# Performance work log

Hardware: AMD Instinct MI355X
Metric: run time of the kernel (lower is better)

## Reference

```python
import jax, jax.numpy as jnp
import numpy as np

N, B, E = 50000, 1, 800000
D_IN = 128      # input_size == out_size (residual)
HID = 128       # hidden_size
H = 4           # heads
C = HID // H    # per-head dim = 32
EPS = 1e-5


def setup_inputs() -> dict:
    key = jax.random.key(0)
    ks = jax.random.split(key, 16)
    s_in = 1.0 / np.sqrt(D_IN)
    s_hid = 1.0 / np.sqrt(HID)
    return {
        "x": jax.random.normal(ks[0], (N, B, D_IN), jnp.float32),
        "edge_index": jax.random.randint(ks[1], (2, E), 0, N, jnp.int64 if jax.config.jax_enable_x64 else jnp.int32),
        "edge_attr": jax.random.normal(ks[2], (E, HID), jnp.float32),
        # TransformerConv projections (weights stored torch-style [out, in])
        "Wq": jax.random.uniform(ks[3], (HID, D_IN), jnp.float32, -s_in, s_in),
        "bq": jnp.zeros((HID,), jnp.float32),
        "Wk": jax.random.uniform(ks[4], (HID, D_IN), jnp.float32, -s_in, s_in),
        "bk": jnp.zeros((HID,), jnp.float32),
        "Wv": jax.random.uniform(ks[5], (HID, D_IN), jnp.float32, -s_in, s_in),
        "bv": jnp.zeros((HID,), jnp.float32),
        "We": jax.random.uniform(ks[6], (HID, HID), jnp.float32, -s_hid, s_hid),  # lin_edge, no bias
        "Wskip": jax.random.uniform(ks[7], (HID, D_IN), jnp.float32, -s_in, s_in),
        "bskip": jnp.zeros((HID,), jnp.float32),
        "Wp": jax.random.uniform(ks[8], (HID, HID), jnp.float32, -s_hid, s_hid),   # physics_linear
        "bp": jnp.zeros((HID,), jnp.float32),
        "Wm": jax.random.uniform(ks[9], (D_IN, HID), jnp.float32, -s_hid, s_hid),  # merge_linear
        "bm": jnp.zeros((D_IN,), jnp.float32),
    }


def reference(x, edge_index, edge_attr, Wq, bq, Wk, bk, Wv, bv, We,
              Wskip, bskip, Wp, bp, Wm, bm):
    n = x.shape[0]
    src, dst = edge_index[0], edge_index[1]  # message flows src -> dst (j -> i)

    # node-wise QKV projections -> [N, B, H, C]
    q = (x @ Wq.T + bq).reshape(n, B, H, C)
    k = (x @ Wk.T + bk).reshape(n, B, H, C)
    v = (x @ Wv.T + bv).reshape(n, B, H, C)

    # edge feature projection -> [E, H, C]
    e = (edge_attr @ We.T).reshape(-1, H, C)

    # per-edge attention scores [E, B, H]
    k_j = k[src] + e[:, None]                       # [E, B, H, C]
    alpha = (q[dst] * k_j).sum(-1) / jnp.sqrt(jnp.asarray(C, x.dtype))

    # scatter-softmax over incoming edges of each dst node
    m = jax.ops.segment_max(alpha, dst, num_segments=n)      # [N, B, H]
    a = jnp.exp(alpha - m[dst])
    s = jax.ops.segment_sum(a, dst, num_segments=n)
    alpha = a / s[dst]

    # weighted scatter-add aggregation
    msg = (v[src] + e[:, None]) * alpha[..., None]           # [E, B, H, C]
    out = jax.ops.segment_sum(msg, dst, num_segments=n)      # [N, B, H, C]
    out = out.reshape(n, B, H * C)

    # root skip connection
    out = out + (x @ Wskip.T + bskip)

    # GraphResidualBlock tail
    out = jax.nn.relu(out)
    out = out @ Wp.T + bp
    # custom LayerNorm: normalize over the node dim (dim 0), weight/bias unused
    mu = out.mean(0, keepdims=True)
    sd = out.std(0, keepdims=True)
    out = (out - mu) / (sd + EPS)
    out = jax.nn.relu(out)
    out = out @ Wm.T + bm
    return out + x
```

## Files before the change

### kernel.cpp

```cpp
#include <hip/hip_runtime.h>
#include <stdint.h>

#define RS32 0.17677669529663687f
#define LDW 40

typedef short bf16x8 __attribute__((ext_vector_type(8)));
typedef float f32x4 __attribute__((ext_vector_type(4)));

__device__ __forceinline__ ushort f2bf(float f) {
  uint32_t b = __float_as_uint(f);
  b = (b + 0x7fffu + ((b >> 16) & 1u)) >> 16;
  return (ushort)b;
}
__device__ __forceinline__ float bflo(uint32_t w) { return __uint_as_float(w << 16); }
__device__ __forceinline__ float bfhi(uint32_t w) { return __uint_as_float(w & 0xffff0000u); }

__device__ __forceinline__ void stage16(ushort* hiA, ushort* loA, int r, int koff,
                                        const float* v) {
  uint32_t hu[8], lu[8];
#pragma unroll
  for (int i = 0; i < 8; ++i) {
    uint32_t b0 = __float_as_uint(v[2 * i]), b1 = __float_as_uint(v[2 * i + 1]);
    uint32_t h0m = b0 & 0xffff0000u, h1m = b1 & 0xffff0000u;
    hu[i] = (b0 >> 16) | h1m;
    float l0 = v[2 * i] - __uint_as_float(h0m);
    float l1 = v[2 * i + 1] - __uint_as_float(h1m);
    lu[i] = (__float_as_uint(l0) >> 16) | (__float_as_uint(l1) & 0xffff0000u);
  }
  *(uint4*)&hiA[r * LDW + koff]     = make_uint4(hu[0], hu[1], hu[2], hu[3]);
  *(uint4*)&hiA[r * LDW + koff + 8] = make_uint4(hu[4], hu[5], hu[6], hu[7]);
  *(uint4*)&loA[r * LDW + koff]     = make_uint4(lu[0], lu[1], lu[2], lu[3]);
  *(uint4*)&loA[r * LDW + koff + 8] = make_uint4(lu[4], lu[5], lu[6], lu[7]);
}

__launch_bounds__(256)
__global__ void gemm128_mfma_kernel(int mode,
                                    const float* __restrict__ A, const float* __restrict__ A2,
                                    const float* __restrict__ W, const float* __restrict__ bias,
                                    const float* __restrict__ mu, const float* __restrict__ inv,
                                    const float* __restrict__ X, float* __restrict__ out,
                                    float* __restrict__ sums, float* __restrict__ sumsq, int N)
{
  __shared__ ushort Ahi[128 * LDW], Alo[128 * LDW], Whi[128 * LDW], Wlo[128 * LDW];
  const int tid = threadIdx.x;
  const int nb = blockIdx.x * 128;
  const int lane = tid & 63, wv = tid >> 6;
  const int wr = (wv >> 1) * 64, wc = (wv & 1) * 64;
  const int fr = lane & 15, fq = lane >> 4;
  const int sr = tid >> 1, sk = (tid & 1) * 16;

  f32x4 acc[4][4];
#pragma unroll
  for (int m = 0; m < 4; ++m)
#pragma unroll
    for (int n = 0; n < 4; ++n) acc[m][n] = (f32x4)0.0f;

  for (int kc = 0; kc < 128; kc += 32) {
    float va[16], vw[16];
    {
      int gr = nb + sr;
      if (gr < N) {
#pragma unroll
        for (int i = 0; i < 4; ++i) {
          float4 v = *(const float4*)(A + (size_t)gr * 128 + kc + sk + i * 4);
          if (mode == 1) {
            float4 b = *(const float4*)(A2 + (size_t)gr * 128 + kc + sk + i * 4);
            v.x = fmaxf(v.x + b.x, 0.f); v.y = fmaxf(v.y + b.y, 0.f);
            v.z = fmaxf(v.z + b.z, 0.f); v.w = fmaxf(v.w + b.w, 0.f);
          } else if (mode == 2) {
            float4 m4 = *(const float4*)(mu + kc + sk + i * 4);
            float4 i4 = *(const float4*)(inv + kc + sk + i * 4);
            v.x = fmaxf((v.x - m4.x) * i4.x, 0.f); v.y = fmaxf((v.y - m4.y) * i4.y, 0.f);
            v.z = fmaxf((v.z - m4.z) * i4.z, 0.f); v.w = fmaxf((v.w - m4.w) * i4.w, 0.f);
          }
          va[i * 4 + 0] = v.x; va[i * 4 + 1] = v.y; va[i * 4 + 2] = v.z; va[i * 4 + 3] = v.w;
        }
      } else {
#pragma unroll
        for (int i = 0; i < 16; ++i) va[i] = 0.f;
      }
#pragma unroll
      for (int i = 0; i < 4; ++i) {
        float4 v = *(const float4*)(W + (size_t)sr * 128 + kc + sk + i * 4);
        vw[i * 4 + 0] = v.x; vw[i * 4 + 1] = v.y; vw[i * 4 + 2] = v.z; vw[i * 4 + 3] = v.w;
      }
    }
    if (kc) __syncthreads();
    stage16(Ahi, Alo, sr, sk, va);
    stage16(Whi, Wlo, sr, sk, vw);
    __syncthreads();

    bf16x8 ah[4], al[4], bh[4], bl[4];
#pragma unroll
    for (int m = 0; m < 4; ++m) {
      const int row = wr + m * 16 + fr;
      ah[m] = *(const bf16x8*)&Ahi[row * LDW + fq * 8];
      al[m] = *(const bf16x8*)&Alo[row * LDW + fq * 8];
    }
#pragma unroll
    for (int n = 0; n < 4; ++n) {
      const int col = wc + n * 16 + fr;
      bh[n] = *(const bf16x8*)&Whi[col * LDW + fq * 8];
      bl[n] = *(const bf16x8*)&Wlo[col * LDW + fq * 8];
    }
#pragma unroll
    for (int m = 0; m < 4; ++m)
#pragma unroll
      for (int n = 0; n < 4; ++n) {
        acc[m][n] = __builtin_amdgcn_mfma_f32_16x16x32_bf16(ah[m], bh[n], acc[m][n], 0, 0, 0);
        acc[m][n] = __builtin_amdgcn_mfma_f32_16x16x32_bf16(al[m], bh[n], acc[m][n], 0, 0, 0);
        acc[m][n] = __builtin_amdgcn_mfma_f32_16x16x32_bf16(ah[m], bl[n], acc[m][n], 0, 0, 0);
      }
  }

  float bcol[4];
#pragma unroll
  for (int n = 0; n < 4; ++n) bcol[n] = bias[wc + n * 16 + fr];
  float csum[4] = {0.f, 0.f, 0.f, 0.f}, csum2[4] = {0.f, 0.f, 0.f, 0.f};
#pragma unroll
  for (int m = 0; m < 4; ++m) {
    const int r0 = nb + wr + m * 16 + fq * 4;
#pragma unroll
    for (int r = 0; r < 4; ++r) {
      const int gr = r0 + r;
      if (gr < N) {
#pragma unroll
        for (int n = 0; n < 4; ++n) {
          const int c = wc + n * 16 + fr;
          float o = acc[m][n][r] + bcol[n];
          if (mode == 2) o += X[(size_t)gr * 128 + c];
          out[(size_t)gr * 128 + c] = o;
          if (mode == 1) { csum[n] += o; csum2[n] = fmaf(o, o, csum2[n]); }
        }
      }
    }
  }
  if (mode == 1) {
#pragma unroll
    for (int n = 0; n < 4; ++n) {
      csum[n] += __shfl_xor(csum[n], 16, 64);
      csum[n] += __shfl_xor(csum[n], 32, 64);
      csum2[n] += __shfl_xor(csum2[n], 16, 64);
      csum2[n] += __shfl_xor(csum2[n], 32, 64);
    }
    if (fq == 0) {
#pragma unroll
      for (int n = 0; n < 4; ++n) {
        atomicAdd(&sums[wc + n * 16 + fr], csum[n]);
        atomicAdd(&sumsq[wc + n * 16 + fr], csum2[n]);
      }
    }
  }
}

__launch_bounds__(256)
__global__ void proj_direct_kernel(const ushort* __restrict__ xb16,
                                   const ushort* __restrict__ Wb,
                                   const ushort* __restrict__ Mtb,
                                   const float* __restrict__ bk, const float* __restrict__ bv,
                                   const float* __restrict__ bs, const float* __restrict__ bq,
                                   const float* __restrict__ bu,
                                   float* __restrict__ os, ushort* __restrict__ kvi,
                                   ushort* __restrict__ u, ushort* __restrict__ qb, int N)
{
  const int y = blockIdx.y;
  const ushort* Wsrc = (y < 4) ? (Wb + (size_t)y * 16384) : (Mtb + (size_t)(y - 4) * 16384);

  const int tid = threadIdx.x;
  const int nb = blockIdx.x * 128;
  const int lane = tid & 63, wv = tid >> 6;
  const int wr = (wv >> 1) * 64, wc = (wv & 1) * 64;
  const int fr = lane & 15, fq = lane >> 4;

  f32x4 acc[4][4];
#pragma unroll
  for (int m = 0; m < 4; ++m)
#pragma unroll
    for (int n = 0; n < 4; ++n) acc[m][n] = (f32x4)0.0f;

#pragma unroll
  for (int kk = 0; kk < 4; ++kk) {
    const int ko = kk * 32 + fq * 8;
    bf16x8 af[4], bf[4];
#pragma unroll
    for (int m = 0; m < 4; ++m)
      af[m] = *(const bf16x8*)(xb16 + (size_t)(nb + wr + m * 16 + fr) * 128 + ko);
#pragma unroll
    for (int n = 0; n < 4; ++n)
      bf[n] = *(const bf16x8*)(Wsrc + (size_t)(wc + n * 16 + fr) * 128 + ko);
#pragma unroll
    for (int m = 0; m < 4; ++m)
#pragma unroll
      for (int n = 0; n < 4; ++n)
        acc[m][n] = __builtin_amdgcn_mfma_f32_16x16x32_bf16(af[m], bf[n], acc[m][n], 0, 0, 0);
  }

  float bcol[4];
#pragma unroll
  for (int n = 0; n < 4; ++n) {
    const int c = wc + n * 16 + fr;
    bcol[n] = (y == 0) ? bk[c] : (y == 1) ? bv[c] : (y == 2) ? bs[c]
            : (y == 3) ? bq[c] : bu[(y - 4) * 128 + c];
  }
#pragma unroll
  for (int m = 0; m < 4; ++m) {
    const int r0 = nb + wr + m * 16 + fq * 4;
#pragma unroll
    for (int r = 0; r < 4; ++r) {
      const int gr = r0 + r;
      if (gr < N) {
#pragma unroll
        for (int n = 0; n < 4; ++n) {
          const int c = wc + n * 16 + fr;
          float o = acc[m][n][r] + bcol[n];
          if (y == 2)      os[(size_t)gr * 128 + c] = o;
          else if (y == 3) qb[(size_t)gr * 128 + c] = f2bf(o);
          else if (y == 0) kvi[(size_t)gr * 256 + (c >> 2) * 8 + (c & 3)] = f2bf(o);
          else if (y == 1) kvi[(size_t)gr * 256 + (c >> 2) * 8 + 4 + (c & 3)] = f2bf(o);
          else             u[(size_t)gr * 512 + (y - 4) * 128 + c] = f2bf(o);
        }
      }
    }
  }
}

__global__ void x2bf_kernel(const float* __restrict__ x, ushort* __restrict__ xb, int total4)
{
  int i = blockIdx.x * 256 + threadIdx.x;
  if (i < total4) {
    float4 v = ((const float4*)x)[i];
    uint2 w = make_uint2((uint32_t)f2bf(v.x) | ((uint32_t)f2bf(v.y) << 16),
                         (uint32_t)f2bf(v.z) | ((uint32_t)f2bf(v.w) << 16));
    ((uint2*)xb)[i] = w;
  }
}

__global__ void prep_wb_kernel(const float* __restrict__ Wk, const float* __restrict__ Wv,
                               const float* __restrict__ Ws, const float* __restrict__ Wq,
                               ushort* __restrict__ Wb)
{
  int i = blockIdx.x * 256 + threadIdx.x;
  if (i >= 4 * 16384) return;
  int y = i >> 14, r = i & 16383;
  const float* src = (y == 0) ? Wk : (y == 1) ? Wv : (y == 2) ? Ws : Wq;
  Wb[i] = f2bf(src[r]);
}

__global__ void prep_mt_kernel(const float* __restrict__ Wq, const float* __restrict__ We,
                               ushort* __restrict__ Mtb)
{
  const int tid = threadIdx.x;
  const int jp = blockIdx.x * 2 + (tid >> 7);
  const int d = tid & 127;
  const int h = jp >> 7, j = jp & 127;
  const float* wq = Wq + (size_t)(32 * h) * 128 + d;
  const float* we = We + (size_t)(32 * h) * 128 + j;
  float acc = 0.f;
#pragma unroll 8
  for (int a = 0; a < 32; ++a) acc = fmaf(wq[a * 128], we[a * 128], acc);
  Mtb[(size_t)jp * 128 + d] = f2bf(acc);
}

__global__ void prep_bu_kernel(const float* __restrict__ bq, const float* __restrict__ We,
                               float* __restrict__ bu)
{
  const int jp = threadIdx.x;
  const int h = jp >> 7, j = jp & 127;
  float acc = 0.f;
  for (int a = 0; a < 32; ++a)
    acc = fmaf(bq[32 * h + a], We[(size_t)(32 * h + a) * 128 + j], acc);
  bu[jp] = acc;
}

__global__ void prep_web_kernel(const float* __restrict__ We, ushort* __restrict__ WeB)
{
  int idx = blockIdx.x * 256 + threadIdx.x;
  if (idx >= 128 * 512) return;
  int c = idx >> 9, j = idx & 511;
  int hh = j >> 7, k2 = j & 127;
  WeB[idx] = (hh == (c >> 5)) ? f2bf(We[(size_t)c * 128 + k2]) : (ushort)0;
}

__global__ void deg_kernel(const int* __restrict__ ei, int* __restrict__ deg, int E)
{
  int e = blockIdx.x * 256 + threadIdx.x;
  if (e < E) atomicAdd(&deg[ei[E + e]], 1);
}

__launch_bounds__(256)
__global__ void start_kernel(const int* __restrict__ deg, int* __restrict__ offs,
                             int* __restrict__ cursor, int* __restrict__ gcount, int N)
{
  const int i = blockIdx.x * 256 + threadIdx.x;
  const int lane = threadIdx.x & 63;
  int d = (i < N) ? deg[i] : 0;
  int scan = d;
#pragma unroll
  for (int ofs = 1; ofs < 64; ofs <<= 1) {
    int t = __shfl_up(scan, ofs, 64);
    if (lane >= ofs) scan += t;
  }
  int total = __shfl(scan, 63, 64);
  int base = 0;
  if (lane == 63) base = atomicAdd(gcount, total);
  base = __shfl(base, 63, 64);
  int excl = base + scan - d;
  if (i < N) { offs[i] = excl; cursor[i] = excl; }
}

__global__ void fill_kernel(const int* __restrict__ ei, int* __restrict__ cursor,
                            int2* __restrict__ csr, int E)
{
  int e = blockIdx.x * 256 + threadIdx.x;
  if (e < E) {
    int dst = ei[E + e];
    int slot = atomicAdd(&cursor[dst], 1);
    csr[slot] = make_int2(ei[e], e);
  }
}

__launch_bounds__(256)
__global__ void fused_attn2_kernel(const int2* __restrict__ csr, const int* __restrict__ offs,
                                   const int* __restrict__ deg,
                                   const ushort* __restrict__ qb, const ushort* __restrict__ kvi,
                                   const ushort* __restrict__ u,
                                   const float* __restrict__ eattr,
                                   ushort* __restrict__ aggS, float* __restrict__ wsS, int N)
{
  const int tid = threadIdx.x;
  const int lane = tid & 63;
  const int wid = tid >> 6;
  const int p = lane >> 5;
  const int j32 = lane & 31;
  const int c0 = j32 * 4;
  const int h = j32 >> 3;
  const int gwave = blockIdx.x * 4 + wid;
  const int nwaves = gridDim.x * 4;

  for (int n = gwave; n < N; n += nwaves) {
    const int e0 = offs[n];
    const int e1 = e0 + deg[n];

    const uint2 qp = *(const uint2*)(qb + (size_t)n * 128 + c0);
    uint2 uhp[4];
#pragma unroll
    for (int hh = 0; hh < 4; ++hh)
      uhp[hh] = *(const uint2*)(u + (size_t)n * 512 + hh * 128 + c0);

    float ws0 = 0.f, ws1 = 0.f, ws2 = 0.f, ws3 = 0.f;
    float ax[4][4];
#pragma unroll
    for (int hh = 0; hh < 4; ++hh)
#pragma unroll
      for (int j = 0; j < 4; ++j) ax[hh][j] = 0.f;
    float sm0 = 0.f, sm1 = 0.f, sm2 = 0.f, sm3 = 0.f;

    int sl = e0 + p;
    if (sl < e1) {
      int2 seC = csr[sl];
      float4 eaC = *(const float4*)(eattr + (size_t)seC.y * 128 + c0);
      uint4 kvC = *(const uint4*)(kvi + (size_t)seC.x * 256 + j32 * 8);
      int sln = sl + 2;
      int2 seN = (sln < e1) ? csr[sln] : seC;
      for (; sl < e1; sl += 2) {
        float4 eaN = *(const float4*)(eattr + (size_t)seN.y * 128 + c0);
        uint4 kvN = *(const uint4*)(kvi + (size_t)seN.x * 256 + j32 * 8);
        const int slf = sl + 4;
        int2 seF = (slf < e1) ? csr[slf] : seN;

        float P0 = eaC.x * bflo(uhp[0].x) + eaC.y * bfhi(uhp[0].x)
                 + eaC.z * bflo(uhp[0].y) + eaC.w * bfhi(uhp[0].y);
        float P1 = eaC.x * bflo(uhp[1].x) + eaC.y * bfhi(uhp[1].x)
                 + eaC.z * bflo(uhp[1].y) + eaC.w * bfhi(uhp[1].y);
        float P2 = eaC.x * bflo(uhp[2].x) + eaC.y * bfhi(uhp[2].x)
                 + eaC.z * bflo(uhp[2].y) + eaC.w * bfhi(uhp[2].y);
        float P3 = eaC.x * bflo(uhp[3].x) + eaC.y * bfhi(uhp[3].x)
                 + eaC.z * bflo(uhp[3].y) + eaC.w * bfhi(uhp[3].y);
        const float qk = bflo(qp.x) * bflo(kvC.x) + bfhi(qp.x) * bfhi(kvC.x)
                       + bflo(qp.y) * bflo(kvC.y) + bfhi(qp.y) * bfhi(kvC.y);
        P0 += (h == 0) ? qk : 0.f;
        P1 += (h == 1) ? qk : 0.f;
        P2 += (h == 2) ? qk : 0.f;
        P3 += (h == 3) ? qk : 0.f;
#pragma unroll
        for (int mm = 1; mm <= 16; mm <<= 1) {
          P0 += __shfl_xor(P0, mm, 64);
          P1 += __shfl_xor(P1, mm, 64);
          P2 += __shfl_xor(P2, mm, 64);
          P3 += __shfl_xor(P3, mm, 64);
        }
        const float a0 = __expf(P0 * RS32);
        const float a1 = __expf(P1 * RS32);
        const float a2 = __expf(P2 * RS32);
        const float a3 = __expf(P3 * RS32);
        sm0 += a0; sm1 += a1; sm2 += a2; sm3 += a3;
        const float aV = (h == 0) ? a0 : (h == 1) ? a1 : (h == 2) ? a2 : a3;
        ws0 = fmaf(aV, bflo(kvC.z), ws0); ws1 = fmaf(aV, bfhi(kvC.z), ws1);
        ws2 = fmaf(aV, bflo(kvC.w), ws2); ws3 = fmaf(aV, bfhi(kvC.w), ws3);
        ax[0][0] = fmaf(a0, eaC.x, ax[0][0]); ax[0][1] = fmaf(a0, eaC.y, ax[0][1]);
        ax[0][2] = fmaf(a0, eaC.z, ax[0][2]); ax[0][3] = fmaf(a0, eaC.w, ax[0][3]);
        ax[1][0] = fmaf(a1, eaC.x, ax[1][0]); ax[1][1] = fmaf(a1, eaC.y, ax[1][1]);
        ax[1][2] = fmaf(a1, eaC.z, ax[1][2]); ax[1][3] = fmaf(a1, eaC.w, ax[1][3]);
        ax[2][0] = fmaf(a2, eaC.x, ax[2][0]); ax[2][1] = fmaf(a2, eaC.y, ax[2][1]);
        ax[2][2] = fmaf(a2, eaC.z, ax[2][2]); ax[2][3] = fmaf(a2, eaC.w, ax[2][3]);
        ax[3][0] = fmaf(a3, eaC.x, ax[3][0]); ax[3][1] = fmaf(a3, eaC.y, ax[3][1]);
        ax[3][2] = fmaf(a3, eaC.z, ax[3][2]); ax[3][3] = fmaf(a3, eaC.w, ax[3][3]);

        eaC = eaN; kvC = kvN; seN = seF;
      }
    }

#pragma unroll
    for (int hh = 0; hh < 4; ++hh)
#pragma unroll
      for (int j = 0; j < 4; ++j) ax[hh][j] += __shfl_xor(ax[hh][j], 32, 64);
    ws0 += __shfl_xor(ws0, 32, 64); ws1 += __shfl_xor(ws1, 32, 64);
    ws2 += __shfl_xor(ws2, 32, 64); ws3 += __shfl_xor(ws3, 32, 64);
    sm0 += __shfl_xor(sm0, 32, 64); sm1 += __shfl_xor(sm1, 32, 64);
    sm2 += __shfl_xor(sm2, 32, 64); sm3 += __shfl_xor(sm3, 32, 64);

    const float iv0 = (sm0 > 0.f) ? 1.f / sm0 : 0.f;
    const float iv1 = (sm1 > 0.f) ? 1.f / sm1 : 0.f;
    const float iv2 = (sm2 > 0.f) ? 1.f / sm2 : 0.f;
    const float iv3 = (sm3 > 0.f) ? 1.f / sm3 : 0.f;

    if (p == 0) {
      const float s = (h == 0) ? iv0 : (h == 1) ? iv1 : (h == 2) ? iv2 : iv3;
      *(float4*)(wsS + (size_t)n * 128 + c0) =
          make_float4(ws0 * s, ws1 * s, ws2 * s, ws3 * s);
    }

    float o0[4], o1[4], s0, s1;
    if (p == 0) {
#pragma unroll
      for (int j = 0; j < 4; ++j) { o0[j] = ax[0][j]; o1[j] = ax[1][j]; }
      s0 = iv0; s1 = iv1;
    } else {
#pragma unroll
      for (int j = 0; j < 4; ++j) { o0[j] = ax[2][j]; o1[j] = ax[3][j]; }
      s0 = iv2; s1 = iv3;
    }
    uint2 w0 = make_uint2(((uint32_t)f2bf(o0[0] * s0)) | (((uint32_t)f2bf(o0[1] * s0)) << 16),
                          ((uint32_t)f2bf(o0[2] * s0)) | (((uint32_t)f2bf(o0[3] * s0)) << 16));
    uint2 w1 = make_uint2(((uint32_t)f2bf(o1[0] * s1)) | (((uint32_t)f2bf(o1[1] * s1)) << 16),
                          ((uint32_t)f2bf(o1[2] * s1)) | (((uint32_t)f2bf(o1[3] * s1)) << 16));
    *(uint2*)(aggS + (size_t)n * 512 + (p * 2) * 128 + c0) = w0;
    *(uint2*)(aggS + (size_t)n * 512 + (p * 2 + 1) * 128 + c0) = w1;
  }
}

__launch_bounds__(256)
__global__ void agg_gemm_kernel(const ushort* __restrict__ aggS, const ushort* __restrict__ WeB,
                                const float* __restrict__ wsX, float* __restrict__ attn, int N)
{
  __shared__ ushort As[128][72];
  __shared__ ushort Bs[128][72];
  const int tid = threadIdx.x;
  const int nb = blockIdx.x * 128;
  const int lane = tid & 63, wv = tid >> 6;
  const int wr = (wv >> 1) * 64, wc = (wv & 1) * 64;
  const int fr = lane & 15, fq = lane >> 4;
  const int r = tid >> 1, cs = (tid & 1) * 32;

  f32x4 acc[4][4];
#pragma unroll
  for (int m = 0; m < 4; ++m)
#pragma unroll
    for (int n = 0; n < 4; ++n) acc[m][n] = (f32x4)0.0f;

  for (int kc = 0; kc < 512; kc += 64) {
    uint4 av[4], bv[4];
    if (nb + r < N) {
      const uint4* src = (const uint4*)(aggS + (size_t)(nb + r) * 512 + kc + cs);
      av[0] = src[0]; av[1] = src[1]; av[2] = src[2]; av[3] = src[3];
    } else {
#pragma unroll
      for (int i = 0; i < 4; ++i) av[i] = make_uint4(0, 0, 0, 0);
    }
    {
      const uint4* src = (const uint4*)(WeB + (size_t)r * 512 + kc + cs);
      bv[0] = src[0]; bv[1] = src[1]; bv[2] = src[2]; bv[3] = src[3];
    }
    if (kc) __syncthreads();
#pragma unroll
    for (int i = 0; i < 4; ++i) {
      *(uint4*)&As[r][cs + i * 8] = av[i];
      *(uint4*)&Bs[r][cs + i * 8] = bv[i];
    }
    __syncthreads();

#pragma unroll
    for (int s = 0; s < 2; ++s) {
      bf16x8 ah[4], bh[4];
#pragma unroll
      for (int m = 0; m < 4; ++m)
        ah[m] = *(const bf16x8*)&As[wr + m * 16 + fr][s * 32 + fq * 8];
#pragma unroll
      for (int n = 0; n < 4; ++n)
        bh[n] = *(const bf16x8*)&Bs[wc + n * 16 + fr][s * 32 + fq * 8];
#pragma unroll
      for (int m = 0; m < 4; ++m)
#pragma unroll
        for (int n = 0; n < 4; ++n)
          acc[m][n] = __builtin_amdgcn_mfma_f32_16x16x32_bf16(ah[m], bh[n], acc[m][n], 0, 0, 0);
    }
  }

#pragma unroll
  for (int m = 0; m < 4; ++m) {
    const int r0 = nb + wr + m * 16 + fq * 4;
#pragma unroll
    for (int rr = 0; rr < 4; ++rr) {
      const int gr = r0 + rr;
      if (gr < N) {
#pragma unroll
        for (int n = 0; n < 4; ++n) {
          const int c = wc + n * 16 + fr;
          attn[(size_t)gr * 128 + c] = acc[m][n][rr] + wsX[(size_t)gr * 128 + c];
        }
      }
    }
  }
}

__global__ void finalize_stats_kernel(const float* __restrict__ sums, const float* __restrict__ sumsq,
                                      float* __restrict__ mu, float* __restrict__ inv, int N)
{
  int c = threadIdx.x;
  float m = sums[c] / (float)N;
  float var = sumsq[c] / (float)N - m * m;
  float sd = sqrtf(fmaxf(var, 0.f));
  mu[c] = m;
  inv[c] = 1.f / (sd + 1e-5f);
}

extern "C" void kernel_launch(void* const* d_in, const int* in_sizes, int n_in,
                              void* d_out, int out_size, void* d_ws, size_t ws_size,
                              hipStream_t stream) {
  const float* x    = (const float*)d_in[0];
  const int*   ei   = (const int*)d_in[1];
  const float* eatt = (const float*)d_in[2];
  const float* Wq = (const float*)d_in[3];  const float* bq = (const float*)d_in[4];
  const float* Wk = (const float*)d_in[5];  const float* bk = (const float*)d_in[6];
  const float* Wv = (const float*)d_in[7];  const float* bv = (const float*)d_in[8];
  const float* We = (const float*)d_in[9];
  const float* Wsk = (const float*)d_in[10]; const float* bsk = (const float*)d_in[11];
  const float* Wp = (const float*)d_in[12]; const float* bp = (const float*)d_in[13];
  const float* Wm = (const float*)d_in[14]; const float* bm = (const float*)d_in[15];
  float* out = (float*)d_out;

  const int N = in_sizes[0] / 128;
  const int E = in_sizes[1] / 2;

  char* w = (char*)d_ws;
  auto alloc = [&](size_t bytes) {
    char* p = w;
    w += (bytes + 255) & ~(size_t)255;
    return p;
  };
  const size_t node_f = (size_t)N * 128 * sizeof(float);
  float*  skip = (float*)alloc(node_f);
  float*  wsA  = (float*)alloc(node_f);
  float*  t1   = (float*)alloc(node_f);
  ushort* xb16 = (ushort*)alloc((size_t)N * 128 * sizeof(ushort));
  ushort* qb   = (ushort*)alloc((size_t)N * 128 * sizeof(ushort));
  ushort* kvi  = (ushort*)alloc((size_t)N * 256 * sizeof(ushort));
  ushort* u    = (ushort*)alloc((size_t)N * 512 * sizeof(ushort));
  ushort* aggS = (ushort*)alloc((size_t)N * 512 * sizeof(ushort));
  ushort* WeB  = (ushort*)alloc(128 * 512 * sizeof(ushort));
  ushort* Wb   = (ushort*)alloc(4 * 128 * 128 * sizeof(ushort));
  ushort* Mtb  = (ushort*)alloc(512 * 128 * sizeof(ushort));
  float*  bu   = (float*)alloc(512 * sizeof(float));
  int*    deg  = (int*)alloc((size_t)N * sizeof(int));
  int*    offs = (int*)alloc((size_t)N * sizeof(int));
  int*    curs = (int*)alloc((size_t)N * sizeof(int));
  int*    gcnt = (int*)alloc(sizeof(int));
  int2*   csr  = (int2*)alloc((size_t)E * sizeof(int2));
  float*  sums  = (float*)alloc(128 * sizeof(float));
  float*  sumsq = (float*)alloc(128 * sizeof(float));
  float*  mu    = (float*)alloc(128 * sizeof(float));
  float*  inv   = (float*)alloc(128 * sizeof(float));
  (void)ws_size; (void)n_in; (void)out_size;

  const int NB = (N + 127) / 128;
  const int EB = (E + 255) / 256;

  hipMemsetAsync(deg, 0, (size_t)N * sizeof(int), stream);
  hipMemsetAsync(gcnt, 0, sizeof(int), stream);
  hipMemsetAsync(sums, 0, 2 * 128 * sizeof(float), stream);

  x2bf_kernel<<<(N * 32 + 255) / 256, 256, 0, stream>>>(x, xb16, N * 32);
  prep_wb_kernel<<<256, 256, 0, stream>>>(Wk, Wv, Wsk, Wq, Wb);
  prep_mt_kernel<<<256, 256, 0, stream>>>(Wq, We, Mtb);
  prep_bu_kernel<<<1, 512, 0, stream>>>(bq, We, bu);
  prep_web_kernel<<<256, 256, 0, stream>>>(We, WeB);

  proj_direct_kernel<<<dim3(NB, 8), 256, 0, stream>>>(xb16, Wb, Mtb, bk, bv, bsk, bq, bu,
                                                      skip, kvi, u, qb, N);

  deg_kernel<<<EB, 256, 0, stream>>>(ei, deg, E);
  start_kernel<<<(N + 255) / 256, 256, 0, stream>>>(deg, offs, curs, gcnt, N);
  fill_kernel<<<EB, 256, 0, stream>>>(ei, curs, csr, E);

  fused_attn2_kernel<<<2048, 256, 0, stream>>>(csr, offs, deg, qb, kvi, u, eatt,
                                               aggS, wsA, N);

  agg_gemm_kernel<<<NB, 256, 0, stream>>>(aggS, WeB, wsA, wsA, N);

  gemm128_mfma_kernel<<<NB, 256, 0, stream>>>(1, wsA, skip, Wp, bp, nullptr, nullptr, nullptr,
                                              t1, sums, sumsq, N);
  finalize_stats_kernel<<<1, 128, 0, stream>>>(sums, sumsq, mu, inv, N);

  gemm128_mfma_kernel<<<NB, 256, 0, stream>>>(2, t1, nullptr, Wm, bm, mu, inv, x, out,
                                              nullptr, nullptr, N);
}
```

Measured before the change: 517.7 us.

## Fuse aggregation GEMM with physics linear and drop split-bf16 tail GEMMs

Fuses the edge-aggregation GEMM with the residual add, skip add, ReLU and the physics_linear GEMM plus column statistics into one kernel. The ReLU output stays in shared memory, so the float intermediate never round-trips through global memory. The skip projection is now stored as bf16. The tail GEMMs drop the hi/lo split-bf16 three-MFMA scheme for a single bf16 MFMA, with a separate kernel that normalizes and casts the second input to bf16. This cuts memory traffic and MFMA work at the cost of lower precision (plain bf16 operands) in the tail.

```diff
diff --git a/kernel.cpp b/kernel.cpp
--- a/kernel.cpp
+++ b/kernel.cpp
@@ -2,7 +2,6 @@
 #include <stdint.h>
 
 #define RS32 0.17677669529663687f
-#define LDW 40
 
 typedef short bf16x8 __attribute__((ext_vector_type(8)));
 typedef float f32x4 __attribute__((ext_vector_type(4)));
@@ -14,144 +13,7 @@
 }
 __device__ __forceinline__ float bflo(uint32_t w) { return __uint_as_float(w << 16); }
 __device__ __forceinline__ float bfhi(uint32_t w) { return __uint_as_float(w & 0xffff0000u); }
-
-__device__ __forceinline__ void stage16(ushort* hiA, ushort* loA, int r, int koff,
-                                        const float* v) {
-  uint32_t hu[8], lu[8];
-#pragma unroll
-  for (int i = 0; i < 8; ++i) {
-    uint32_t b0 = __float_as_uint(v[2 * i]), b1 = __float_as_uint(v[2 * i + 1]);
-    uint32_t h0m = b0 & 0xffff0000u, h1m = b1 & 0xffff0000u;
-    hu[i] = (b0 >> 16) | h1m;
-    float l0 = v[2 * i] - __uint_as_float(h0m);
-    float l1 = v[2 * i + 1] - __uint_as_float(h1m);
-    lu[i] = (__float_as_uint(l0) >> 16) | (__float_as_uint(l1) & 0xffff0000u);
-  }
-  *(uint4*)&hiA[r * LDW + koff]     = make_uint4(hu[0], hu[1], hu[2], hu[3]);
-  *(uint4*)&hiA[r * LDW + koff + 8] = make_uint4(hu[4], hu[5], hu[6], hu[7]);
-  *(uint4*)&loA[r * LDW + koff]     = make_uint4(lu[0], lu[1], lu[2], lu[3]);
-  *(uint4*)&loA[r * LDW + koff + 8] = make_uint4(lu[4], lu[5], lu[6], lu[7]);
-}
-
-__launch_bounds__(256)
-__global__ void gemm128_mfma_kernel(int mode,
-                                    const float* __restrict__ A, const float* __restrict__ A2,
-                                    const float* __restrict__ W, const float* __restrict__ bias,
-                                    const float* __restrict__ mu, const float* __restrict__ inv,
-                                    const float* __restrict__ X, float* __restrict__ out,
-                                    float* __restrict__ sums, float* __restrict__ sumsq, int N)
-{
-  __shared__ ushort Ahi[128 * LDW], Alo[128 * LDW], Whi[128 * LDW], Wlo[128 * LDW];
-  const int tid = threadIdx.x;
-  const int nb = blockIdx.x * 128;
-  const int lane = tid & 63, wv = tid >> 6;
-  const int wr = (wv >> 1) * 64, wc = (wv & 1) * 64;
-  const int fr = lane & 15, fq = lane >> 4;
-  const int sr = tid >> 1, sk = (tid & 1) * 16;
-
-  f32x4 acc[4][4];
-#pragma unroll
-  for (int m = 0; m < 4; ++m)
-#pragma unroll
-    for (int n = 0; n < 4; ++n) acc[m][n] = (f32x4)0.0f;
-
-  for (int kc = 0; kc < 128; kc += 32) {
-    float va[16], vw[16];
-    {
-      int gr = nb + sr;
-      if (gr < N) {
-#pragma unroll
-        for (int i = 0; i < 4; ++i) {
-          float4 v = *(const float4*)(A + (size_t)gr * 128 + kc + sk + i * 4);
-          if (mode == 1) {
-            float4 b = *(const float4*)(A2 + (size_t)gr * 128 + kc + sk + i * 4);
-            v.x = fmaxf(v.x + b.x, 0.f); v.y = fmaxf(v.y + b.y, 0.f);
-            v.z = fmaxf(v.z + b.z, 0.f); v.w = fmaxf(v.w + b.w, 0.f);
-          } else if (mode == 2) {
-            float4 m4 = *(const float4*)(mu + kc + sk + i * 4);
-            float4 i4 = *(const float4*)(inv + kc + sk + i * 4);
-            v.x = fmaxf((v.x - m4.x) * i4.x, 0.f); v.y = fmaxf((v.y - m4.y) * i4.y, 0.f);
-            v.z = fmaxf((v.z - m4.z) * i4.z, 0.f); v.w = fmaxf((v.w - m4.w) * i4.w, 0.f);
-          }
-          va[i * 4 + 0] = v.x; va[i * 4 + 1] = v.y; va[i * 4 + 2] = v.z; va[i * 4 + 3] = v.w;
-        }
-      } else {
-#pragma unroll
-        for (int i = 0; i < 16; ++i) va[i] = 0.f;
-      }
-#pragma unroll
-      for (int i = 0; i < 4; ++i) {
-        float4 v = *(const float4*)(W + (size_t)sr * 128 + kc + sk + i * 4);
-        vw[i * 4 + 0] = v.x; vw[i * 4 + 1] = v.y; vw[i * 4 + 2] = v.z; vw[i * 4 + 3] = v.w;
-      }
-    }
-    if (kc) __syncthreads();
-    stage16(Ahi, Alo, sr, sk, va);
-    stage16(Whi, Wlo, sr, sk, vw);
-    __syncthreads();
-
-    bf16x8 ah[4], al[4], bh[4], bl[4];
-#pragma unroll
-    for (int m = 0; m < 4; ++m) {
-      const int row = wr + m * 16 + fr;
-      ah[m] = *(const bf16x8*)&Ahi[row * LDW + fq * 8];
-      al[m] = *(const bf16x8*)&Alo[row * LDW + fq * 8];
-    }
-#pragma unroll
-    for (int n = 0; n < 4; ++n) {
-      const int col = wc + n * 16 + fr;
-      bh[n] = *(const bf16x8*)&Whi[col * LDW + fq * 8];
-      bl[n] = *(const bf16x8*)&Wlo[col * LDW + fq * 8];
-    }
-#pragma unroll
-    for (int m = 0; m < 4; ++m)
-#pragma unroll
-      for (int n = 0; n < 4; ++n) {
-        acc[m][n] = __builtin_amdgcn_mfma_f32_16x16x32_bf16(ah[m], bh[n], acc[m][n], 0, 0, 0);
-        acc[m][n] = __builtin_amdgcn_mfma_f32_16x16x32_bf16(al[m], bh[n], acc[m][n], 0, 0, 0);
-        acc[m][n] = __builtin_amdgcn_mfma_f32_16x16x32_bf16(ah[m], bl[n], acc[m][n], 0, 0, 0);
-      }
-  }
-
-  float bcol[4];
-#pragma unroll
-  for (int n = 0; n < 4; ++n) bcol[n] = bias[wc + n * 16 + fr];
-  float csum[4] = {0.f, 0.f, 0.f, 0.f}, csum2[4] = {0.f, 0.f, 0.f, 0.f};
-#pragma unroll
-  for (int m = 0; m < 4; ++m) {
-    const int r0 = nb + wr + m * 16 + fq * 4;
-#pragma unroll
-    for (int r = 0; r < 4; ++r) {
-      const int gr = r0 + r;
-      if (gr < N) {
-#pragma unroll
-        for (int n = 0; n < 4; ++n) {
-          const int c = wc + n * 16 + fr;
-          float o = acc[m][n][r] + bcol[n];
-          if (mode == 2) o += X[(size_t)gr * 128 + c];
-          out[(size_t)gr * 128 + c] = o;
-          if (mode == 1) { csum[n] += o; csum2[n] = fmaf(o, o, csum2[n]); }
-        }
-      }
-    }
-  }
-  if (mode == 1) {
-#pragma unroll
-    for (int n = 0; n < 4; ++n) {
-      csum[n] += __shfl_xor(csum[n], 16, 64);
-      csum[n] += __shfl_xor(csum[n], 32, 64);
-      csum2[n] += __shfl_xor(csum2[n], 16, 64);
-      csum2[n] += __shfl_xor(csum2[n], 32, 64);
-    }
-    if (fq == 0) {
-#pragma unroll
-      for (int n = 0; n < 4; ++n) {
-        atomicAdd(&sums[wc + n * 16 + fr], csum[n]);
-        atomicAdd(&sumsq[wc + n * 16 + fr], csum2[n]);
-      }
-    }
-  }
-}
+__device__ __forceinline__ float bfu(ushort s) { return __uint_as_float(((uint32_t)s) << 16); }
 
 __launch_bounds__(256)
 __global__ void proj_direct_kernel(const ushort* __restrict__ xb16,
@@ -160,7 +22,7 @@
                                    const float* __restrict__ bk, const float* __restrict__ bv,
                                    const float* __restrict__ bs, const float* __restrict__ bq,
                                    const float* __restrict__ bu,
-                                   float* __restrict__ os, ushort* __restrict__ kvi,
+                                   ushort* __restrict__ skipb, ushort* __restrict__ kvi,
                                    ushort* __restrict__ u, ushort* __restrict__ qb, int N)
 {
   const int y = blockIdx.y;
@@ -213,7 +75,7 @@
         for (int n = 0; n < 4; ++n) {
           const int c = wc + n * 16 + fr;
           float o = acc[m][n][r] + bcol[n];
-          if (y == 2)      os[(size_t)gr * 128 + c] = o;
+          if (y == 2)      skipb[(size_t)gr * 128 + c] = f2bf(o);
           else if (y == 3) qb[(size_t)gr * 128 + c] = f2bf(o);
           else if (y == 0) kvi[(size_t)gr * 256 + (c >> 2) * 8 + (c & 3)] = f2bf(o);
           else if (y == 1) kvi[(size_t)gr * 256 + (c >> 2) * 8 + 4 + (c & 3)] = f2bf(o);
@@ -244,6 +106,13 @@
   int y = i >> 14, r = i & 16383;
   const float* src = (y == 0) ? Wk : (y == 1) ? Wv : (y == 2) ? Ws : Wq;
   Wb[i] = f2bf(src[r]);
+}
+
+__global__ void prep_w2_kernel(const float* __restrict__ Wp, const float* __restrict__ Wm,
+                               ushort* __restrict__ Wpb, ushort* __restrict__ Wmb)
+{
+  int i = blockIdx.x * 256 + threadIdx.x;
+  if (i < 16384) { Wpb[i] = f2bf(Wp[i]); Wmb[i] = f2bf(Wm[i]); }
 }
 
 __global__ void prep_mt_kernel(const float* __restrict__ Wq, const float* __restrict__ We,
@@ -450,11 +319,15 @@
 }
 
 __launch_bounds__(256)
-__global__ void agg_gemm_kernel(const ushort* __restrict__ aggS, const ushort* __restrict__ WeB,
-                                const float* __restrict__ wsX, float* __restrict__ attn, int N)
-{
-  __shared__ ushort As[128][72];
-  __shared__ ushort Bs[128][72];
+__global__ void fused_post_kernel(const ushort* __restrict__ aggS, const ushort* __restrict__ WeB,
+                                  const float* __restrict__ wsS, const ushort* __restrict__ skipb,
+                                  const ushort* __restrict__ Wpb, const float* __restrict__ bp,
+                                  float* __restrict__ t1,
+                                  float* __restrict__ sums, float* __restrict__ sumsq, int N)
+{
+  __shared__ ushort smem[2 * 128 * 72];
+  ushort* As = smem;
+  ushort* Bs = smem + 128 * 72;
   const int tid = threadIdx.x;
   const int nb = blockIdx.x * 128;
   const int lane = tid & 63, wv = tid >> 6;
@@ -484,8 +357,8 @@
     if (kc) __syncthreads();
 #pragma unroll
     for (int i = 0; i < 4; ++i) {
-      *(uint4*)&As[r][cs + i * 8] = av[i];
-      *(uint4*)&Bs[r][cs + i * 8] = bv[i];
+      *(uint4*)&As[r * 72 + cs + i * 8] = av[i];
+      *(uint4*)&Bs[r * 72 + cs + i * 8] = bv[i];
     }
     __syncthreads();
 
@@ -494,10 +367,10 @@
       bf16x8 ah[4], bh[4];
 #pragma unroll
       for (int m = 0; m < 4; ++m)
-        ah[m] = *(const bf16x8*)&As[wr + m * 16 + fr][s * 32 + fq * 8];
+        ah[m] = *(const bf16x8*)&As[(wr + m * 16 + fr) * 72 + s * 32 + fq * 8];
 #pragma unroll
       for (int n = 0; n < 4; ++n)
-        bh[n] = *(const bf16x8*)&Bs[wc + n * 16 + fr][s * 32 + fq * 8];
+        bh[n] = *(const bf16x8*)&Bs[(wc + n * 16 + fr) * 72 + s * 32 + fq * 8];
 #pragma unroll
       for (int m = 0; m < 4; ++m)
 #pragma unroll
@@ -505,7 +378,56 @@
           acc[m][n] = __builtin_amdgcn_mfma_f32_16x16x32_bf16(ah[m], bh[n], acc[m][n], 0, 0, 0);
     }
   }
-
+  __syncthreads();
+
+  ushort* zs = smem;
+#pragma unroll
+  for (int m = 0; m < 4; ++m) {
+    const int lr0 = wr + m * 16 + fq * 4;
+#pragma unroll
+    for (int rr = 0; rr < 4; ++rr) {
+      const int lrow = lr0 + rr;
+      const int gr = nb + lrow;
+#pragma unroll
+      for (int n = 0; n < 4; ++n) {
+        const int c = wc + n * 16 + fr;
+        float o = 0.f;
+        if (gr < N) {
+          o = acc[m][n][rr] + wsS[(size_t)gr * 128 + c] + bfu(skipb[(size_t)gr * 128 + c]);
+          o = fmaxf(o, 0.f);
+        }
+        zs[lrow * 136 + c] = f2bf(o);
+      }
+    }
+  }
+  __syncthreads();
+
+  f32x4 acc2[4][4];
+#pragma unroll
+  for (int m = 0; m < 4; ++m)
+#pragma unroll
+    for (int n = 0; n < 4; ++n) acc2[m][n] = (f32x4)0.0f;
+#pragma unroll
+  for (int kk = 0; kk < 4; ++kk) {
+    const int ko = kk * 32 + fq * 8;
+    bf16x8 af[4], bf[4];
+#pragma unroll
+    for (int m = 0; m < 4; ++m)
+      af[m] = *(const bf16x8*)&zs[(wr + m * 16 + fr) * 136 + ko];
+#pragma unroll
+    for (int n = 0; n < 4; ++n)
+      bf[n] = *(const bf16x8*)(Wpb + (size_t)(wc + n * 16 + fr) * 128 + ko);
+#pragma unroll
+    for (int m = 0; m < 4; ++m)
+#pragma unroll
+      for (int n = 0; n < 4; ++n)
+        acc2[m][n] = __builtin_amdgcn_mfma_f32_16x16x32_bf16(af[m], bf[n], acc2[m][n], 0, 0, 0);
+  }
+
+  float bcol[4];
+#pragma unroll
+  for (int n = 0; n < 4; ++n) bcol[n] = bp[wc + n * 16 + fr];
+  float csum[4] = {0.f, 0.f, 0.f, 0.f}, csum2[4] = {0.f, 0.f, 0.f, 0.f};
 #pragma unroll
   for (int m = 0; m < 4; ++m) {
     const int r0 = nb + wr + m * 16 + fq * 4;
@@ -516,9 +438,25 @@
 #pragma unroll
         for (int n = 0; n < 4; ++n) {
           const int c = wc + n * 16 + fr;
-          attn[(size_t)gr * 128 + c] = acc[m][n][rr] + wsX[(size_t)gr * 128 + c];
+          float o = acc2[m][n][rr] + bcol[n];
+          t1[(size_t)gr * 128 + c] = o;
+          csum[n] += o; csum2[n] = fmaf(o, o, csum2[n]);
         }
       }
+    }
+  }
+#pragma unroll
+  for (int n = 0; n < 4; ++n) {
+    csum[n] += __shfl_xor(csum[n], 16, 64);
+    csum[n] += __shfl_xor(csum[n], 32, 64);
+    csum2[n] += __shfl_xor(csum2[n], 16, 64);
+    csum2[n] += __shfl_xor(csum2[n], 32, 64);
+  }
+  if (fq == 0) {
+#pragma unroll
+    for (int n = 0; n < 4; ++n) {
+      atomicAdd(&sums[wc + n * 16 + fr], csum[n]);
+      atomicAdd(&sumsq[wc + n * 16 + fr], csum2[n]);
     }
   }
 }
@@ -532,6 +470,79 @@
   float sd = sqrtf(fmaxf(var, 0.f));
   mu[c] = m;
   inv[c] = 1.f / (sd + 1e-5f);
+}
+
+__global__ void z2_kernel(const float* __restrict__ t1, const float* __restrict__ mu,
+                          const float* __restrict__ inv, ushort* __restrict__ zb, int total4)
+{
+  int i = blockIdx.x * 256 + threadIdx.x;
+  if (i < total4) {
+    const int c0 = (i & 31) * 4;
+    float4 v = ((const float4*)t1)[i];
+    float4 m4 = *(const float4*)(mu + c0);
+    float4 i4 = *(const float4*)(inv + c0);
+    float z0 = fmaxf((v.x - m4.x) * i4.x, 0.f);
+    float z1 = fmaxf((v.y - m4.y) * i4.y, 0.f);
+    float z2v = fmaxf((v.z - m4.z) * i4.z, 0.f);
+    float z3 = fmaxf((v.w - m4.w) * i4.w, 0.f);
+    uint2 w = make_uint2((uint32_t)f2bf(z0) | ((uint32_t)f2bf(z1) << 16),
+                         (uint32_t)f2bf(z2v) | ((uint32_t)f2bf(z3) << 16));
+    ((uint2*)zb)[i] = w;
+  }
+}
+
+__launch_bounds__(256)
+__global__ void out_gemm_kernel(const ushort* __restrict__ zb, const ushort* __restrict__ Wmb,
+                                const float* __restrict__ bm, const float* __restrict__ x,
+                                float* __restrict__ out, int N)
+{
+  const int tid = threadIdx.x;
+  const int nb = blockIdx.x * 128;
+  const int lane = tid & 63, wv = tid >> 6;
+  const int wr = (wv >> 1) * 64, wc = (wv & 1) * 64;
+  const int fr = lane & 15, fq = lane >> 4;
+
+  f32x4 acc[4][4];
+#pragma unroll
+  for (int m = 0; m < 4; ++m)
+#pragma unroll
+    for (int n = 0; n < 4; ++n) acc[m][n] = (f32x4)0.0f;
+
+#pragma unroll
+  for (int kk = 0; kk < 4; ++kk) {
+    const int ko = kk * 32 + fq * 8;
+    bf16x8 af[4], bf[4];
+#pragma unroll
+    for (int m = 0; m < 4; ++m)
+      af[m] = *(const bf16x8*)(zb + (size_t)(nb + wr + m * 16 + fr) * 128 + ko);
+#pragma unroll
+    for (int n = 0; n < 4; ++n)
+      bf[n] = *(const bf16x8*)(Wmb + (size_t)(wc + n * 16 + fr) * 128 + ko);
+#pragma unroll
+    for (int m = 0; m < 4; ++m)
+#pragma unroll
+      for (int n = 0; n < 4; ++n)
+        acc[m][n] = __builtin_amdgcn_mfma_f32_16x16x32_bf16(af[m], bf[n], acc[m][n], 0, 0, 0);
+  }
+
+  float bcol[4];
+#pragma unroll
+  for (int n = 0; n < 4; ++n) bcol[n] = bm[wc + n * 16 + fr];
+#pragma unroll
+  for (int m = 0; m < 4; ++m) {
+    const int r0 = nb + wr + m * 16 + fq * 4;
+#pragma unroll
+    for (int r = 0; r < 4; ++r) {
+      const int gr = r0 + r;
+      if (gr < N) {
+#pragma unroll
+        for (int n = 0; n < 4; ++n) {
+          const int c = wc + n * 16 + fr;
+          out[(size_t)gr * 128 + c] = acc[m][n][r] + bcol[n] + x[(size_t)gr * 128 + c];
+        }
+      }
+    }
+  }
 }
 
 extern "C" void kernel_launch(void* const* d_in, const int* in_sizes, int n_in,
@@ -559,17 +570,20 @@
     return p;
   };
   const size_t node_f = (size_t)N * 128 * sizeof(float);
-  float*  skip = (float*)alloc(node_f);
   float*  wsA  = (float*)alloc(node_f);
   float*  t1   = (float*)alloc(node_f);
   ushort* xb16 = (ushort*)alloc((size_t)N * 128 * sizeof(ushort));
+  ushort* skipb= (ushort*)alloc((size_t)N * 128 * sizeof(ushort));
   ushort* qb   = (ushort*)alloc((size_t)N * 128 * sizeof(ushort));
+  ushort* zb   = (ushort*)alloc((size_t)N * 128 * sizeof(ushort));
   ushort* kvi  = (ushort*)alloc((size_t)N * 256 * sizeof(ushort));
   ushort* u    = (ushort*)alloc((size_t)N * 512 * sizeof(ushort));
   ushort* aggS = (ushort*)alloc((size_t)N * 512 * sizeof(ushort));
   ushort* WeB  = (ushort*)alloc(128 * 512 * sizeof(ushort));
   ushort* Wb   = (ushort*)alloc(4 * 128 * 128 * sizeof(ushort));
   ushort* Mtb  = (ushort*)alloc(512 * 128 * sizeof(ushort));
+  ushort* Wpb  = (ushort*)alloc(128 * 128 * sizeof(ushort));
+  ushort* Wmb  = (ushort*)alloc(128 * 128 * sizeof(ushort));
   float*  bu   = (float*)alloc(512 * sizeof(float));
   int*    deg  = (int*)alloc((size_t)N * sizeof(int));
   int*    offs = (int*)alloc((size_t)N * sizeof(int));
@@ -591,12 +605,13 @@
 
   x2bf_kernel<<<(N * 32 + 255) / 256, 256, 0, stream>>>(x, xb16, N * 32);
   prep_wb_kernel<<<256, 256, 0, stream>>>(Wk, Wv, Wsk, Wq, Wb);
+  prep_w2_kernel<<<64, 256, 0, stream>>>(Wp, Wm, Wpb, Wmb);
   prep_mt_kernel<<<256, 256, 0, stream>>>(Wq, We, Mtb);
   prep_bu_kernel<<<1, 512, 0, stream>>>(bq, We, bu);
   prep_web_kernel<<<256, 256, 0, stream>>>(We, WeB);
 
   proj_direct_kernel<<<dim3(NB, 8), 256, 0, stream>>>(xb16, Wb, Mtb, bk, bv, bsk, bq, bu,
-                                                      skip, kvi, u, qb, N);
+                                                      skipb, kvi, u, qb, N);
 
   deg_kernel<<<EB, 256, 0, stream>>>(ei, deg, E);
   start_kernel<<<(N + 255) / 256, 256, 0, stream>>>(deg, offs, curs, gcnt, N);
@@ -605,12 +620,10 @@
   fused_attn2_kernel<<<2048, 256, 0, stream>>>(csr, offs, deg, qb, kvi, u, eatt,
                                                aggS, wsA, N);
 
-  agg_gemm_kernel<<<NB, 256, 0, stream>>>(aggS, WeB, wsA, wsA, N);
-
-  gemm128_mfma_kernel<<<NB, 256, 0, stream>>>(1, wsA, skip, Wp, bp, nullptr, nullptr, nullptr,
-                                              t1, sums, sumsq, N);
+  fused_post_kernel<<<NB, 256, 0, stream>>>(aggS, WeB, wsA, skipb, Wpb, bp,
+                                            t1, sums, sumsq, N);
   finalize_stats_kernel<<<1, 128, 0, stream>>>(sums, sumsq, mu, inv, N);
 
-  gemm128_mfma_kernel<<<NB, 256, 0, stream>>>(2, t1, nullptr, Wm, bm, mu, inv, x, out,
-                                              nullptr, nullptr, N);
-}
+  z2_kernel<<<(N * 32 + 255) / 256, 256, 0, stream>>>(t1, mu, inv, zb, N * 32);
+  out_gemm_kernel<<<NB, 256, 0, stream>>>(zb, Wmb, bm, x, out, N);
+}
```

After: 479.4 us. -7.4%, faster.
